# Optimization experiments

Hardware: AMD Instinct MI355X
Metric: run time of the kernel (lower is better)

Reference implementation:

```python
import jax, jax.numpy as jnp
import numpy as np

N, D, E, EDGE_DIM, HID4 = 8192, 128, 262144, 50, 32


def setup_inputs() -> dict:
    key = jax.random.key(0)
    k = jax.random.split(key, 8)
    return {
        "mag": jax.random.uniform(k[0], (N, D), dtype=jnp.float32),
        "phase": jax.random.normal(k[1], (N, D), dtype=jnp.float32),
        "edge_index": jax.random.randint(k[2], (2, E), 0, N, dtype=jnp.int64),
        "rbf": jax.random.uniform(k[3], (E, EDGE_DIM), dtype=jnp.float32),
        "W1": jax.random.normal(k[4], (EDGE_DIM, HID4), dtype=jnp.float32) * 0.1,
        "b1": jnp.zeros((HID4,), dtype=jnp.float32),
        "W2": jax.random.normal(k[5], (HID4, 1), dtype=jnp.float32) * 0.1,
        "b2": jnp.zeros((1,), dtype=jnp.float32),
    }


def reference(mag, phase, edge_index, rbf, W1, b1, W2, b2):
    # score_ij = sum_d |z_i||z_j| cos(theta_i - theta_j) / sqrt(D)
    # cos(a-b) identity: = (mag*cos(phase)) @ (mag*cos(phase))^T + (mag*sin)@(mag*sin)^T
    scale = jnp.sqrt(jnp.asarray(mag.shape[-1], mag.dtype))
    a = mag * jnp.cos(phase)  # [N, D]
    b = mag * jnp.sin(phase)  # [N, D]
    scores = (a @ a.T + b @ b.T) / scale  # [N, N]
    # edge bias: Linear -> SiLU -> Linear -> scalar, scattered onto (i, j)
    h = jax.nn.silu(rbf @ W1 + b1)       # [E, HID4]
    bias = (h @ W2 + b2)[:, 0]           # [E]
    scores = scores.at[edge_index[0], edge_index[1]].add(bias)
    attn = jax.nn.softmax(scores, axis=1)  # softmax over keys j
    new_mag = attn @ mag
    new_phase = attn @ phase
    return new_mag, new_phase
```

## Files before the change

### kernel.cpp

```cpp
#include <hip/hip_runtime.h>
#include <hip/hip_bf16.h>

#define NN 8192
#define DD 128
#define DQK 256
#define EE 262144
#define EDGE_DIM 50
#define HID 32
#define CAP 96
#define SCALE 0.08838834764831845f
#define SCALE_LOG2E 0.12752455522410585f

using f32x4 = __attribute__((ext_vector_type(4))) float;
using f32x2 = __attribute__((ext_vector_type(2))) float;
using bf16x8 = __attribute__((ext_vector_type(8))) short;
using s16x4 = __attribute__((ext_vector_type(4))) short;

static __device__ __forceinline__ short f2b(float f) {
  __hip_bfloat16 h = __float2bfloat16(f);
  return __builtin_bit_cast(short, h);
}
static __device__ __forceinline__ float b2f(short s) {
  unsigned u = ((unsigned)(unsigned short)s) << 16;
  return __builtin_bit_cast(float, u);
}
static __device__ __forceinline__ void gll(const short* g, short* l) {
  __builtin_amdgcn_global_load_lds(
      (const __attribute__((address_space(1))) void*)g,
      (__attribute__((address_space(3))) void*)l, 16, 0, 0);
}

__global__ __launch_bounds__(256) void k1_mega(
    const float* __restrict__ mag, const float* __restrict__ phase,
    short* __restrict__ qkb, short* __restrict__ vtb, short* __restrict__ vb16,
    const float* __restrict__ rbf, const float* __restrict__ W1,
    const float* __restrict__ b1, const float* __restrict__ W2,
    const float* __restrict__ b2, const int* __restrict__ eidx,
    float* __restrict__ bias, int* __restrict__ cnt, int* __restrict__ slot) {
  __shared__ float tile[64][65];
  int b = blockIdx.x;
  int tid = threadIdx.x;
  if (b < 4096) {
    int t = b * 256 + tid;
    int n = t >> 7, d = t & 127;
    float m = mag[t], p = phase[t];
    float sn, cs;
    __sincosf(p, &sn, &cs);
    qkb[(size_t)n * DQK + d] = f2b(m * cs);
    qkb[(size_t)n * DQK + 128 + d] = f2b(m * sn);
    vb16[(size_t)n * DQK + d] = f2b(m);
    vb16[(size_t)n * DQK + 128 + d] = f2b(p);
    return;
  }
  if (b < 4608) {
    int r = b - 4096;
    int bn = r & 127, bd = (r >> 7) & 1, sel = r >> 8;
    const float* src = sel ? phase : mag;
#pragma unroll
    for (int rep = 0; rep < 16; ++rep) {
      int idx = rep * 256 + tid;
      int rr = idx >> 6, c = idx & 63;
      tile[rr][c] = src[(size_t)(bn * 64 + rr) * DD + bd * 64 + c];
    }
    __syncthreads();
#pragma unroll
    for (int rep = 0; rep < 16; ++rep) {
      int idx = rep * 256 + tid;
      int rr = idx >> 6, c = idx & 63;
      vtb[(size_t)(sel * 128 + bd * 64 + rr) * NN + bn * 64 + c] = f2b(tile[c][rr]);
    }
    return;
  }
  int e = (b - 4608) * 256 + tid;
  const float* rrow = rbf + (size_t)e * EDGE_DIM;
  f32x4 r4[12];
#pragma unroll
  for (int k = 0; k < 12; ++k) r4[k] = *reinterpret_cast<const f32x4*>(rrow + 4 * k);
  f32x2 rt2 = *reinterpret_cast<const f32x2*>(rrow + 48);
  float h[HID];
#pragma unroll
  for (int jj = 0; jj < HID; ++jj) h[jj] = b1[jj];
#pragma unroll
  for (int k = 0; k < 48; ++k) {
    float r = r4[k >> 2][k & 3];
#pragma unroll
    for (int jj = 0; jj < HID; ++jj) h[jj] += r * W1[k * HID + jj];
  }
#pragma unroll
  for (int jj = 0; jj < HID; ++jj)
    h[jj] += rt2.x * W1[48 * HID + jj] + rt2.y * W1[49 * HID + jj];
  float outv = b2[0];
#pragma unroll
  for (int jj = 0; jj < HID; ++jj) {
    float x = h[jj];
    outv += W2[jj] * (x / (1.0f + __expf(-x)));
  }
  bias[e] = outv;
  int i = eidx[e];
  int p = atomicAdd(&cnt[i], 1);
  if (p < CAP) slot[i * CAP + p] = e;
}

constexpr int TBM = 64;
constexpr int TBN = 128;

template <int NSPLIT>
__global__ __launch_bounds__(512, 4) void k5_flash(
    const short* __restrict__ qk,
    const short* __restrict__ vt,
    float* __restrict__ nump,
    float* __restrict__ denp) {
  constexpr int QCOLS = NN / NSPLIT;
  constexpr int NCHUNK = QCOLS / TBN;
  constexpr int GPQ = 8 / NSPLIT;
  __shared__ alignas(16) short Qs[TBM * 256];
  __shared__ alignas(16) short KV[2 * TBN * 64];
  __shared__ alignas(16) short Ps[TBM * 128];
  int b = blockIdx.x;
  int q = (b & 7) / GPQ;
  int rb = (b >> 3) * GPQ + (b & (GPQ - 1));
  int tid = threadIdx.x;
  int w = tid >> 6, lane = tid & 63;
  int wr = w >> 2, wc = w & 3;
  int l15 = lane & 15, quad = lane >> 4;
  int rsw = l15 & 7;
  int wbase = w * 64;
  int r0 = rb * TBM;
  int cbase = q * QCOLS;

#pragma unroll
  for (int p = 0; p < 4; ++p) {
    int idx = p * 512 + tid;
    int row = idx >> 5, gs = idx & 31;
    gll(qk + (size_t)(r0 + row) * DQK + ((gs ^ (row & 7)) * 8),
        &Qs[(p * 512 + wbase) * 8]);
  }

  f32x4 o[2][4] = {};
  float den[2] = {0.f, 0.f};
  __syncthreads();

  for (int ch = 0; ch < NCHUNK; ++ch) {
    int c0 = cbase + ch * TBN;
#pragma unroll
    for (int p = 0; p < 2; ++p) {
      int idx = p * 512 + tid;
      int col = idx >> 3, gs = idx & 7;
      gll(qk + (size_t)(c0 + col) * DQK + ((gs ^ (col & 7)) * 8),
          &KV[(p * 512 + wbase) * 8]);
    }
    __syncthreads();
    f32x4 s[2][2] = {};
#pragma unroll
    for (int bk = 0; bk < 4; ++bk) {
      int buf = bk & 1;
      if (bk < 3) {
        int nb = buf ^ 1;
#pragma unroll
        for (int p = 0; p < 2; ++p) {
          int idx = p * 512 + tid;
          int col = idx >> 3, gs = idx & 7;
          gll(qk + (size_t)(c0 + col) * DQK + (bk + 1) * 64 + ((gs ^ (col & 7)) * 8),
              &KV[nb * 8192 + (p * 512 + wbase) * 8]);
        }
      }
#pragma unroll
      for (int ks = 0; ks < 2; ++ks) {
        int g = ks * 4 + quad;
        bf16x8 a[2], bb[2];
#pragma unroll
        for (int rt = 0; rt < 2; ++rt)
          a[rt] = *(const bf16x8*)&Qs[(wr * 32 + rt * 16 + l15) * 256 +
                                      ((bk * 8 + g) ^ rsw) * 8];
#pragma unroll
        for (int ct = 0; ct < 2; ++ct)
          bb[ct] = *(const bf16x8*)&KV[buf * 8192 + (wc * 32 + ct * 16 + l15) * 64 +
                                       (g ^ rsw) * 8];
#pragma unroll
        for (int rt = 0; rt < 2; ++rt)
#pragma unroll
          for (int ct = 0; ct < 2; ++ct)
            s[ct][rt] = __builtin_amdgcn_mfma_f32_16x16x32_bf16(bb[ct], a[rt],
                                                                s[ct][rt], 0, 0, 0);
      }
      __syncthreads();
    }
#pragma unroll
    for (int p = 0; p < 4; ++p) {
      int idx = p * 512 + tid;
      int feat = idx >> 3, gs = idx & 7;
      gll(vt + (size_t)feat * NN + c0 + ((gs ^ (feat & 7)) * 8),
          &KV[(p * 512 + wbase) * 8]);
    }
#pragma unroll
    for (int rt = 0; rt < 2; ++rt) {
      int row = wr * 32 + rt * 16 + l15;
#pragma unroll
      for (int ct = 0; ct < 2; ++ct) {
        s16x4 pk;
#pragma unroll
        for (int r = 0; r < 4; ++r) {
          float pv = exp2f(s[ct][rt][r] * SCALE_LOG2E);
          den[rt] += pv;
          pk[r] = f2b(pv);
        }
        int cg = wc * 4 + ct * 2 + (quad >> 1);
        *reinterpret_cast<s16x4*>(
            &Ps[row * 128 + ((cg ^ (row & 7)) * 8 + (quad & 1) * 4)]) = pk;
      }
    }
    __syncthreads();
#pragma unroll
    for (int jb = 0; jb < 2; ++jb) {
      if (jb == 1) {
        __syncthreads();
#pragma unroll
        for (int p = 0; p < 4; ++p) {
          int idx = p * 512 + tid;
          int feat = idx >> 3, gs = idx & 7;
          gll(vt + (size_t)feat * NN + c0 + 64 + ((gs ^ (feat & 7)) * 8),
              &KV[(p * 512 + wbase) * 8]);
        }
        __syncthreads();
      }
#pragma unroll
      for (int ks = 0; ks < 2; ++ks) {
        int g = ks * 4 + quad;
        bf16x8 pa[2], vb[4];
#pragma unroll
        for (int rt = 0; rt < 2; ++rt) {
          int row = wr * 32 + rt * 16 + l15;
          pa[rt] = *(const bf16x8*)&Ps[row * 128 +
                                       (((jb * 8 + g) ^ (row & 7)) * 8)];
        }
#pragma unroll
        for (int ft = 0; ft < 4; ++ft)
          vb[ft] = *(const bf16x8*)&KV[(wc * 64 + ft * 16 + l15) * 64 + (g ^ rsw) * 8];
#pragma unroll
        for (int rt = 0; rt < 2; ++rt)
#pragma unroll
          for (int ft = 0; ft < 4; ++ft)
            o[rt][ft] = __builtin_amdgcn_mfma_f32_16x16x32_bf16(pa[rt], vb[ft],
                                                                o[rt][ft], 0, 0, 0);
      }
    }
    __syncthreads();
  }
  float* npB = nump + (size_t)q * NN * DQK;
#pragma unroll
  for (int rt = 0; rt < 2; ++rt)
#pragma unroll
    for (int ft = 0; ft < 4; ++ft) {
      int row = r0 + wr * 32 + rt * 16 + quad * 4;
      int feat = wc * 64 + ft * 16 + l15;
#pragma unroll
      for (int r = 0; r < 4; ++r)
        npB[(size_t)(row + r) * DQK + feat] = o[rt][ft][r];
    }
  float* dl = reinterpret_cast<float*>(KV);
#pragma unroll
  for (int rt = 0; rt < 2; ++rt) {
    float d = den[rt];
    d += __shfl_xor(d, 16);
    d += __shfl_xor(d, 32);
    if (lane < 16) dl[wc * TBM + wr * 32 + rt * 16 + lane] = d;
  }
  __syncthreads();
  if (tid < TBM) {
    float d = dl[0 * TBM + tid] + dl[1 * TBM + tid] + dl[2 * TBM + tid] +
              dl[3 * TBM + tid];
    denp[q * NN + r0 + tid] = d;
  }
}

__global__ __launch_bounds__(64) void k6_combine(
    const int* __restrict__ eidx, const float* __restrict__ bias,
    const int* __restrict__ cntArr, const int* __restrict__ slot,
    const short* __restrict__ qk, const short* __restrict__ vb16,
    const float* __restrict__ nump, const float* __restrict__ denp,
    float* __restrict__ out, int nsplit) {
  __shared__ short qs[DQK];
  __shared__ int js[CAP];
  __shared__ float bs[CAP];
  __shared__ float ess[CAP];
  __shared__ int keepf[CAP];
  __shared__ float ncl[2][32][8];
  __shared__ float dcl[2];
  int i = blockIdx.x;
  int lane = threadIdx.x;
  int cnt = cntArr[i];
  if (cnt > CAP) cnt = CAP;
  *reinterpret_cast<s16x4*>(&qs[lane * 4]) =
      *reinterpret_cast<const s16x4*>(qk + (size_t)i * DQK + lane * 4);
  for (int p = lane; p < cnt; p += 64) {
    int e = slot[i * CAP + p];
    js[p] = eidx[EE + e];
    bs[p] = bias[e];
  }
  __syncthreads();
  int sub = lane & 7;
  for (int p = lane >> 3; p < cnt; p += 8) {
    int j = js[p];
    const bf16x8* kb = reinterpret_cast<const bf16x8*>(qk + (size_t)j * DQK + sub * 32);
    const bf16x8* qa = reinterpret_cast<const bf16x8*>(qs + sub * 32);
    float sp = 0.f;
#pragma unroll
    for (int t = 0; t < 4; ++t) {
      bf16x8 qv = qa[t];
      bf16x8 kv = kb[t];
#pragma unroll
      for (int u = 0; u < 8; ++u) sp += b2f(qv[u]) * b2f(kv[u]);
    }
    sp += __shfl_xor(sp, 1);
    sp += __shfl_xor(sp, 2);
    sp += __shfl_xor(sp, 4);
    if (sub == 0) ess[p] = __expf(sp * SCALE);
  }
  __syncthreads();
  {
    int myp[2];
    float mybsum[2];
    int mykeep[2];
    int nm = 0;
    for (int p = lane; p < cnt; p += 64) {
      int j = js[p];
      float bsum = bs[p];
      int keep = 1;
      for (int qq = 0; qq < cnt; ++qq) {
        if (qq == p || js[qq] != j) continue;
        if (qq < p) { keep = 0; break; }
        bsum += bs[qq];
      }
      myp[nm] = p; mybsum[nm] = bsum; mykeep[nm] = keep; ++nm;
    }
    __syncthreads();
    for (int k = 0; k < nm; ++k) { bs[myp[k]] = mybsum[k]; keepf[myp[k]] = mykeep[k]; }
    __syncthreads();
  }
  int grp = lane >> 5;
  int l31 = lane & 31;
  f32x4 nc0 = {0.f, 0.f, 0.f, 0.f}, nc1 = {0.f, 0.f, 0.f, 0.f};
  float denc = 0.f;
  for (int p = grp; p < cnt; p += 2) {
    if (!keepf[p]) continue;
    float delta = ess[p] * expm1f(bs[p]);
    denc += delta;
    bf16x8 v = *reinterpret_cast<const bf16x8*>(vb16 + (size_t)js[p] * DQK + l31 * 8);
#pragma unroll
    for (int u = 0; u < 4; ++u) nc0[u] += delta * b2f(v[u]);
#pragma unroll
    for (int u = 0; u < 4; ++u) nc1[u] += delta * b2f(v[4 + u]);
  }
#pragma unroll
  for (int u = 0; u < 4; ++u) {
    ncl[grp][l31][u] = nc0[u];
    ncl[grp][l31][4 + u] = nc1[u];
  }
  if (l31 == 0) dcl[grp] = denc;
  __syncthreads();
  if (grp == 0) {
    float den = dcl[0] + dcl[1];
    f32x4 a0, a1;
#pragma unroll
    for (int u = 0; u < 4; ++u) {
      a0[u] = ncl[0][l31][u] + ncl[1][l31][u];
      a1[u] = ncl[0][l31][4 + u] + ncl[1][l31][4 + u];
    }
    for (int qq = 0; qq < nsplit; ++qq) {
      const float* np = nump + ((size_t)qq * NN + i) * DQK + l31 * 8;
      a0 += *reinterpret_cast<const f32x4*>(np);
      a1 += *reinterpret_cast<const f32x4*>(np + 4);
      den += denp[qq * NN + i];
    }
    float inv = 1.0f / den;
    a0 *= inv;
    a1 *= inv;
    float* dst = (l31 < 16) ? (out + (size_t)i * DD + l31 * 8)
                            : (out + (size_t)NN * DD + (size_t)i * DD + l31 * 8 - 128);
    *reinterpret_cast<f32x4*>(dst) = a0;
    *reinterpret_cast<f32x4*>(dst + 4) = a1;
  }
}

constexpr size_t OFF_QK = 0;
constexpr size_t OFF_VT = (size_t)NN * DQK * 2;
constexpr size_t OFF_VB16 = OFF_VT + (size_t)DQK * NN * 2;
constexpr size_t OFF_BIAS = OFF_VB16 + (size_t)NN * DQK * 2;
constexpr size_t OFF_CNT = OFF_BIAS + (size_t)EE * 4;
constexpr size_t OFF_SLOT = OFF_CNT + (size_t)NN * 4;
constexpr size_t OFF_NUMP = (OFF_SLOT + (size_t)NN * CAP * 4 + 255) & ~(size_t)255;
constexpr size_t WS_NEED4 = OFF_NUMP + 4ull * NN * DQK * 4 + 4ull * NN * 4;
constexpr size_t WS_NEED2 = OFF_NUMP + 2ull * NN * DQK * 4 + 2ull * NN * 4;

extern "C" void kernel_launch(void* const* d_in, const int* in_sizes, int n_in,
                              void* d_out, int out_size, void* d_ws, size_t ws_size,
                              hipStream_t stream) {
  const float* mag = (const float*)d_in[0];
  const float* phase = (const float*)d_in[1];
  const int* eidx = (const int*)d_in[2];
  const float* rbf = (const float*)d_in[3];
  const float* W1 = (const float*)d_in[4];
  const float* b1 = (const float*)d_in[5];
  const float* W2 = (const float*)d_in[6];
  const float* b2 = (const float*)d_in[7];
  float* out = (float*)d_out;
  char* ws = (char*)d_ws;
  if (ws_size < WS_NEED2) return;
  int nsplit = (ws_size >= WS_NEED4) ? 4 : 2;

  short* qkb = (short*)(ws + OFF_QK);
  short* vtb = (short*)(ws + OFF_VT);
  short* vb16 = (short*)(ws + OFF_VB16);
  float* bias = (float*)(ws + OFF_BIAS);
  int* cnt = (int*)(ws + OFF_CNT);
  int* slot = (int*)(ws + OFF_SLOT);
  float* nump = (float*)(ws + OFF_NUMP);
  float* denp = (float*)(ws + OFF_NUMP + (size_t)nsplit * NN * DQK * 4);

  hipMemsetAsync(cnt, 0, (size_t)NN * 4, stream);
  k1_mega<<<5632, 256, 0, stream>>>(mag, phase, qkb, vtb, vb16, rbf, W1, b1, W2,
                                    b2, eidx, bias, cnt, slot);
  if (nsplit == 4)
    k5_flash<4><<<(NN / TBM) * 4, 512, 0, stream>>>(qkb, vtb, nump, denp);
  else
    k5_flash<2><<<(NN / TBM) * 2, 512, 0, stream>>>(qkb, vtb, nump, denp);
  k6_combine<<<NN, 64, 0, stream>>>(eidx, bias, cnt, slot, qkb, vb16, nump, denp,
                                    out, nsplit);
}
```

Before: 261.9 us.

## Split mega prep kernel into three kernels, two edges per MLP thread, wider combine

```diff
diff --git a/kernel.cpp b/kernel.cpp
--- a/kernel.cpp
+++ b/kernel.cpp
@@ -30,75 +30,104 @@
       (__attribute__((address_space(3))) void*)l, 16, 0, 0);
 }
 
-__global__ __launch_bounds__(256) void k1_mega(
+__global__ __launch_bounds__(256) void k1a_prep(
     const float* __restrict__ mag, const float* __restrict__ phase,
-    short* __restrict__ qkb, short* __restrict__ vtb, short* __restrict__ vb16,
+    short* __restrict__ qkb, short* __restrict__ vb16) {
+  int t = blockIdx.x * 256 + threadIdx.x;
+  int n = t >> 7, d = t & 127;
+  float m = mag[t], p = phase[t];
+  float sn, cs;
+  __sincosf(p, &sn, &cs);
+  qkb[(size_t)n * DQK + d] = f2b(m * cs);
+  qkb[(size_t)n * DQK + 128 + d] = f2b(m * sn);
+  vb16[(size_t)n * DQK + d] = f2b(m);
+  vb16[(size_t)n * DQK + 128 + d] = f2b(p);
+}
+
+__global__ __launch_bounds__(256) void k1b_tr(
+    const float* __restrict__ mag, const float* __restrict__ phase,
+    short* __restrict__ vtb) {
+  __shared__ float tile[64][65];
+  int r = blockIdx.x;
+  int tid = threadIdx.x;
+  int bn = r & 127, bd = (r >> 7) & 1, sel = r >> 8;
+  const float* src = sel ? phase : mag;
+#pragma unroll
+  for (int rep = 0; rep < 16; ++rep) {
+    int idx = rep * 256 + tid;
+    int rr = idx >> 6, c = idx & 63;
+    tile[rr][c] = src[(size_t)(bn * 64 + rr) * DD + bd * 64 + c];
+  }
+  __syncthreads();
+#pragma unroll
+  for (int rep = 0; rep < 16; ++rep) {
+    int idx = rep * 256 + tid;
+    int rr = idx >> 6, c = idx & 63;
+    vtb[(size_t)(sel * 128 + bd * 64 + rr) * NN + bn * 64 + c] = f2b(tile[c][rr]);
+  }
+}
+
+__global__ __launch_bounds__(256) void k1c_mlp(
     const float* __restrict__ rbf, const float* __restrict__ W1,
     const float* __restrict__ b1, const float* __restrict__ W2,
     const float* __restrict__ b2, const int* __restrict__ eidx,
     float* __restrict__ bias, int* __restrict__ cnt, int* __restrict__ slot) {
-  __shared__ float tile[64][65];
-  int b = blockIdx.x;
-  int tid = threadIdx.x;
-  if (b < 4096) {
-    int t = b * 256 + tid;
-    int n = t >> 7, d = t & 127;
-    float m = mag[t], p = phase[t];
-    float sn, cs;
-    __sincosf(p, &sn, &cs);
-    qkb[(size_t)n * DQK + d] = f2b(m * cs);
-    qkb[(size_t)n * DQK + 128 + d] = f2b(m * sn);
-    vb16[(size_t)n * DQK + d] = f2b(m);
-    vb16[(size_t)n * DQK + 128 + d] = f2b(p);
-    return;
-  }
-  if (b < 4608) {
-    int r = b - 4096;
-    int bn = r & 127, bd = (r >> 7) & 1, sel = r >> 8;
-    const float* src = sel ? phase : mag;
-#pragma unroll
-    for (int rep = 0; rep < 16; ++rep) {
-      int idx = rep * 256 + tid;
-      int rr = idx >> 6, c = idx & 63;
-      tile[rr][c] = src[(size_t)(bn * 64 + rr) * DD + bd * 64 + c];
-    }
-    __syncthreads();
-#pragma unroll
-    for (int rep = 0; rep < 16; ++rep) {
-      int idx = rep * 256 + tid;
-      int rr = idx >> 6, c = idx & 63;
-      vtb[(size_t)(sel * 128 + bd * 64 + rr) * NN + bn * 64 + c] = f2b(tile[c][rr]);
-    }
-    return;
-  }
-  int e = (b - 4608) * 256 + tid;
-  const float* rrow = rbf + (size_t)e * EDGE_DIM;
-  f32x4 r4[12];
-#pragma unroll
-  for (int k = 0; k < 12; ++k) r4[k] = *reinterpret_cast<const f32x4*>(rrow + 4 * k);
-  f32x2 rt2 = *reinterpret_cast<const f32x2*>(rrow + 48);
-  float h[HID];
-#pragma unroll
-  for (int jj = 0; jj < HID; ++jj) h[jj] = b1[jj];
-#pragma unroll
-  for (int k = 0; k < 48; ++k) {
-    float r = r4[k >> 2][k & 3];
-#pragma unroll
-    for (int jj = 0; jj < HID; ++jj) h[jj] += r * W1[k * HID + jj];
-  }
-#pragma unroll
-  for (int jj = 0; jj < HID; ++jj)
-    h[jj] += rt2.x * W1[48 * HID + jj] + rt2.y * W1[49 * HID + jj];
-  float outv = b2[0];
+  int e0 = blockIdx.x * 512 + threadIdx.x;
+  int e1 = e0 + 256;
+  const float* ra = rbf + (size_t)e0 * EDGE_DIM;
+  const float* rc = rbf + (size_t)e1 * EDGE_DIM;
+  float h0[HID], h1[HID];
 #pragma unroll
   for (int jj = 0; jj < HID; ++jj) {
-    float x = h[jj];
-    outv += W2[jj] * (x / (1.0f + __expf(-x)));
-  }
-  bias[e] = outv;
-  int i = eidx[e];
-  int p = atomicAdd(&cnt[i], 1);
-  if (p < CAP) slot[i * CAP + p] = e;
+    float bb = b1[jj];
+    h0[jj] = bb;
+    h1[jj] = bb;
+  }
+#pragma unroll
+  for (int kb = 0; kb < 6; ++kb) {
+    f32x4 a0 = *reinterpret_cast<const f32x4*>(ra + kb * 8);
+    f32x4 a1 = *reinterpret_cast<const f32x4*>(ra + kb * 8 + 4);
+    f32x4 c0 = *reinterpret_cast<const f32x4*>(rc + kb * 8);
+    f32x4 c1 = *reinterpret_cast<const f32x4*>(rc + kb * 8 + 4);
+#pragma unroll
+    for (int kk = 0; kk < 8; ++kk) {
+      int k = kb * 8 + kk;
+      float wa = (kk < 4) ? a0[kk] : a1[kk - 4];
+      float wb = (kk < 4) ? c0[kk] : c1[kk - 4];
+#pragma unroll
+      for (int jj = 0; jj < HID; ++jj) {
+        float w = W1[k * HID + jj];
+        h0[jj] += wa * w;
+        h1[jj] += wb * w;
+      }
+    }
+  }
+  {
+    f32x2 ta = *reinterpret_cast<const f32x2*>(ra + 48);
+    f32x2 tc = *reinterpret_cast<const f32x2*>(rc + 48);
+#pragma unroll
+    for (int jj = 0; jj < HID; ++jj) {
+      float w48 = W1[48 * HID + jj], w49 = W1[49 * HID + jj];
+      h0[jj] += ta.x * w48 + ta.y * w49;
+      h1[jj] += tc.x * w48 + tc.y * w49;
+    }
+  }
+  float o0 = b2[0], o1 = b2[0];
+#pragma unroll
+  for (int jj = 0; jj < HID; ++jj) {
+    float w = W2[jj];
+    float x0 = h0[jj], x1 = h1[jj];
+    o0 += w * (x0 / (1.0f + __expf(-x0)));
+    o1 += w * (x1 / (1.0f + __expf(-x1)));
+  }
+  bias[e0] = o0;
+  bias[e1] = o1;
+  int i0 = eidx[e0];
+  int p0 = atomicAdd(&cnt[i0], 1);
+  if (p0 < CAP) slot[i0 * CAP + p0] = e0;
+  int i1 = eidx[e1];
+  int p1 = atomicAdd(&cnt[i1], 1);
+  if (p1 < CAP) slot[i1 * CAP + p1] = e1;
 }
 
 constexpr int TBM = 64;
@@ -273,7 +302,7 @@
   }
 }
 
-__global__ __launch_bounds__(64) void k6_combine(
+__global__ __launch_bounds__(128) void k6_combine(
     const int* __restrict__ eidx, const float* __restrict__ bias,
     const int* __restrict__ cntArr, const int* __restrict__ slot,
     const short* __restrict__ qk, const short* __restrict__ vb16,
@@ -284,22 +313,23 @@
   __shared__ float bs[CAP];
   __shared__ float ess[CAP];
   __shared__ int keepf[CAP];
-  __shared__ float ncl[2][32][8];
-  __shared__ float dcl[2];
+  __shared__ float ncl[4][32][8];
+  __shared__ float dcl[4];
   int i = blockIdx.x;
-  int lane = threadIdx.x;
+  int tid = threadIdx.x;
   int cnt = cntArr[i];
   if (cnt > CAP) cnt = CAP;
-  *reinterpret_cast<s16x4*>(&qs[lane * 4]) =
-      *reinterpret_cast<const s16x4*>(qk + (size_t)i * DQK + lane * 4);
-  for (int p = lane; p < cnt; p += 64) {
+  if (tid < 64)
+    *reinterpret_cast<s16x4*>(&qs[tid * 4]) =
+        *reinterpret_cast<const s16x4*>(qk + (size_t)i * DQK + tid * 4);
+  for (int p = tid; p < cnt; p += 128) {
     int e = slot[i * CAP + p];
     js[p] = eidx[EE + e];
     bs[p] = bias[e];
   }
   __syncthreads();
-  int sub = lane & 7;
-  for (int p = lane >> 3; p < cnt; p += 8) {
+  int sub = tid & 7;
+  for (int p = tid >> 3; p < cnt; p += 16) {
     int j = js[p];
     const bf16x8* kb = reinterpret_cast<const bf16x8*>(qk + (size_t)j * DQK + sub * 32);
     const bf16x8* qa = reinterpret_cast<const bf16x8*>(qs + sub * 32);
@@ -318,30 +348,29 @@
   }
   __syncthreads();
   {
-    int myp[2];
-    float mybsum[2];
-    int mykeep[2];
-    int nm = 0;
-    for (int p = lane; p < cnt; p += 64) {
-      int j = js[p];
-      float bsum = bs[p];
-      int keep = 1;
+    int keep = 1;
+    float bsum = 0.f;
+    if (tid < cnt) {
+      int j = js[tid];
+      bsum = bs[tid];
       for (int qq = 0; qq < cnt; ++qq) {
-        if (qq == p || js[qq] != j) continue;
-        if (qq < p) { keep = 0; break; }
+        if (qq == tid || js[qq] != j) continue;
+        if (qq < tid) { keep = 0; break; }
         bsum += bs[qq];
       }
-      myp[nm] = p; mybsum[nm] = bsum; mykeep[nm] = keep; ++nm;
     }
     __syncthreads();
-    for (int k = 0; k < nm; ++k) { bs[myp[k]] = mybsum[k]; keepf[myp[k]] = mykeep[k]; }
+    if (tid < cnt) {
+      bs[tid] = bsum;
+      keepf[tid] = keep;
+    }
     __syncthreads();
   }
-  int grp = lane >> 5;
-  int l31 = lane & 31;
+  int grp = tid >> 5;
+  int l31 = tid & 31;
   f32x4 nc0 = {0.f, 0.f, 0.f, 0.f}, nc1 = {0.f, 0.f, 0.f, 0.f};
   float denc = 0.f;
-  for (int p = grp; p < cnt; p += 2) {
+  for (int p = grp; p < cnt; p += 4) {
     if (!keepf[p]) continue;
     float delta = ess[p] * expm1f(bs[p]);
     denc += delta;
@@ -358,16 +387,17 @@
   }
   if (l31 == 0) dcl[grp] = denc;
   __syncthreads();
-  if (grp == 0) {
-    float den = dcl[0] + dcl[1];
+  if (tid < 32) {
+    float den = dcl[0] + dcl[1] + dcl[2] + dcl[3];
     f32x4 a0, a1;
 #pragma unroll
     for (int u = 0; u < 4; ++u) {
-      a0[u] = ncl[0][l31][u] + ncl[1][l31][u];
-      a1[u] = ncl[0][l31][4 + u] + ncl[1][l31][4 + u];
+      a0[u] = ncl[0][tid][u] + ncl[1][tid][u] + ncl[2][tid][u] + ncl[3][tid][u];
+      a1[u] = ncl[0][tid][4 + u] + ncl[1][tid][4 + u] + ncl[2][tid][4 + u] +
+              ncl[3][tid][4 + u];
     }
     for (int qq = 0; qq < nsplit; ++qq) {
-      const float* np = nump + ((size_t)qq * NN + i) * DQK + l31 * 8;
+      const float* np = nump + ((size_t)qq * NN + i) * DQK + tid * 8;
       a0 += *reinterpret_cast<const f32x4*>(np);
       a1 += *reinterpret_cast<const f32x4*>(np + 4);
       den += denp[qq * NN + i];
@@ -375,8 +405,8 @@
     float inv = 1.0f / den;
     a0 *= inv;
     a1 *= inv;
-    float* dst = (l31 < 16) ? (out + (size_t)i * DD + l31 * 8)
-                            : (out + (size_t)NN * DD + (size_t)i * DD + l31 * 8 - 128);
+    float* dst = (tid < 16) ? (out + (size_t)i * DD + tid * 8)
+                            : (out + (size_t)NN * DD + (size_t)i * DD + tid * 8 - 128);
     *reinterpret_cast<f32x4*>(dst) = a0;
     *reinterpret_cast<f32x4*>(dst + 4) = a1;
   }
@@ -418,12 +448,13 @@
   float* denp = (float*)(ws + OFF_NUMP + (size_t)nsplit * NN * DQK * 4);
 
   hipMemsetAsync(cnt, 0, (size_t)NN * 4, stream);
-  k1_mega<<<5632, 256, 0, stream>>>(mag, phase, qkb, vtb, vb16, rbf, W1, b1, W2,
-                                    b2, eidx, bias, cnt, slot);
+  k1a_prep<<<4096, 256, 0, stream>>>(mag, phase, qkb, vb16);
+  k1b_tr<<<512, 256, 0, stream>>>(mag, phase, vtb);
+  k1c_mlp<<<512, 256, 0, stream>>>(rbf, W1, b1, W2, b2, eidx, bias, cnt, slot);
   if (nsplit == 4)
     k5_flash<4><<<(NN / TBM) * 4, 512, 0, stream>>>(qkb, vtb, nump, denp);
   else
     k5_flash<2><<<(NN / TBM) * 2, 512, 0, stream>>>(qkb, vtb, nump, denp);
-  k6_combine<<<NN, 64, 0, stream>>>(eidx, bias, cnt, slot, qkb, vb16, nump, denp,
-                                    out, nsplit);
-}
+  k6_combine<<<NN, 128, 0, stream>>>(eidx, bias, cnt, slot, qkb, vb16, nump, denp,
+                                     out, nsplit);
+}
```

New measurement: 270.7 us. +3.4%, slower.
